# Kernel optimization log

Hardware: AMD Instinct MI355X
Metric: run time of the kernel (lower is better)

## Reference

```python
import jax, jax.numpy as jnp
import numpy as np

N_P, N_A = 100000, 20000
F_P, D_A, H = 512, 128, 256
E_W, E_C = 200000, 400000


def setup_inputs() -> dict:
    key = jax.random.key(0)
    ks = jax.random.split(key, 32)
    s = 0.05  # param init scale
    inp = {
        # node inputs
        'paper_feat': (jax.random.uniform(ks[0], (N_P, F_P)) < 0.02).astype(jnp.float32),  # sparse multi-hot
        'author_emb': jax.random.normal(ks[1], (N_A, D_A), jnp.float32),
        # edges: author --writes--> paper, paper --cites--> paper
        'writes_src': jax.random.randint(ks[2], (E_W,), 0, N_A, jnp.int32),
        'writes_dst': jax.random.randint(ks[3], (E_W,), 0, N_P, jnp.int32),
        'writes_w': jax.random.uniform(ks[4], (E_W,), jnp.float32),
        'cites_src': jax.random.randint(ks[5], (E_C,), 0, N_P, jnp.int32),
        'cites_dst': jax.random.randint(ks[6], (E_C,), 0, N_P, jnp.int32),
        'cites_w': jax.random.uniform(ks[7], (E_C,), jnp.float32),
        # layer 1 params (in dims per node type: paper=F_P, author=D_A)
        'W1_self_p': jax.random.normal(ks[8], (F_P, H), jnp.float32) * s,
        'b1_self_p': jnp.zeros((H,), jnp.float32),
        'W1_self_a': jax.random.normal(ks[9], (D_A, H), jnp.float32) * s,
        'b1_self_a': jnp.zeros((H,), jnp.float32),
        'W1_rel_writes': jax.random.normal(ks[10], (D_A, H), jnp.float32) * s,
        'b1_rel_writes': jnp.zeros((H,), jnp.float32),
        'W1_rel_cites': jax.random.normal(ks[11], (F_P, H), jnp.float32) * s,
        'b1_rel_cites': jnp.zeros((H,), jnp.float32),
        # layer 2 params (all in dims = H)
        'W2_self_p': jax.random.normal(ks[12], (H, H), jnp.float32) * s,
        'b2_self_p': jnp.zeros((H,), jnp.float32),
        'W2_self_a': jax.random.normal(ks[13], (H, H), jnp.float32) * s,
        'b2_self_a': jnp.zeros((H,), jnp.float32),
        'W2_rel_writes': jax.random.normal(ks[14], (H, H), jnp.float32) * s,
        'b2_rel_writes': jnp.zeros((H,), jnp.float32),
        'W2_rel_cites': jax.random.normal(ks[15], (H, H), jnp.float32) * s,
        'b2_rel_cites': jnp.zeros((H,), jnp.float32),
    }
    return inp


def _hetero_layer(xp, xa, edges, Wsp, bsp, Wsa, bsa, Wrw, brw, Wrc, brc, activation):
    """One HeteroLayer: per-type self linear + per-relation gather/scale/scatter-add."""
    writes_src, writes_dst, writes_w, cites_src, cites_dst, cites_w = edges
    out_p = xp @ Wsp + bsp          # [N_P, H]
    out_a = xa @ Wsa + bsa          # [N_A, H]
    # relation author --writes--> paper
    msg_w = xa @ Wrw + brw          # dense per-relation linear on source nodes
    gathered_w = msg_w[writes_src] * writes_w[:, None]          # gather + edge weight
    out_p = out_p + jax.ops.segment_sum(gathered_w, writes_dst, num_segments=out_p.shape[0])
    # relation paper --cites--> paper
    msg_c = xp @ Wrc + brc
    gathered_c = msg_c[cites_src] * cites_w[:, None]
    out_p = out_p + jax.ops.segment_sum(gathered_c, cites_dst, num_segments=out_p.shape[0])
    if activation:
        out_p = jax.nn.elu(out_p)
        out_a = jax.nn.elu(out_a)
    return out_p, out_a


def reference(paper_feat, author_emb,
              writes_src, writes_dst, writes_w,
              cites_src, cites_dst, cites_w,
              W1_self_p, b1_self_p, W1_self_a, b1_self_a,
              W1_rel_writes, b1_rel_writes, W1_rel_cites, b1_rel_cites,
              W2_self_p, b2_self_p, W2_self_a, b2_self_a,
              W2_rel_writes, b2_rel_writes, W2_rel_cites, b2_rel_cites):
    edges = (writes_src, writes_dst, writes_w, cites_src, cites_dst, cites_w)
    xp, xa = _hetero_layer(paper_feat, author_emb, edges,
                           W1_self_p, b1_self_p, W1_self_a, b1_self_a,
                           W1_rel_writes, b1_rel_writes, W1_rel_cites, b1_rel_cites,
                           activation=True)
    xp, xa = _hetero_layer(xp, xa, edges,
                           W2_self_p, b2_self_p, W2_self_a, b2_self_a,
                           W2_rel_writes, b2_rel_writes, W2_rel_cites, b2_rel_cites,
                           activation=False)
    return xp, xa
```

## Files before the change

kernel.cpp:

```cpp
#include <hip/hip_runtime.h>
#include <cstdint>
#include <cstddef>

constexpr int Hd  = 256;
constexpr int N_P = 100000;
constexpr int N_A = 20000;
constexpr int F_P = 512;
constexpr int D_A = 128;

typedef short bf16x8 __attribute__((ext_vector_type(8)));
typedef float f32x4  __attribute__((ext_vector_type(4)));

__device__ __forceinline__ unsigned short f2b(float x) {
    unsigned u = __float_as_uint(x);
    u += 0x7fffu + ((u >> 16) & 1u);
    return (unsigned short)(u >> 16);
}
__device__ __forceinline__ float b2f(unsigned short h) {
    return __uint_as_float((unsigned)h << 16);
}
__device__ __forceinline__ unsigned pk2(float lo, float hi) {
    return (__float_as_uint(lo) >> 16) | (__float_as_uint(hi) & 0xffff0000u);
}

__device__ __forceinline__ void bsplit(float x, unsigned short& hi, unsigned short& lo) {
    const unsigned u = __float_as_uint(x);
    hi = (unsigned short)(u >> 16);
    const float r = x - __uint_as_float(u & 0xffff0000u);
    lo = (unsigned short)(__float_as_uint(r) >> 16);
}

__global__ void prep_kernel(const float* __restrict__ W1sa, const float* __restrict__ W1rw,
                            const float* __restrict__ W2sa, const float* __restrict__ W2rw,
                            const float* __restrict__ W2rc, const float* __restrict__ W2sp,
                            const float* __restrict__ W1sp, const float* __restrict__ W1rc,
                            const float* __restrict__ b1sa, const float* __restrict__ b1rw,
                            const float* __restrict__ b2sa, const float* __restrict__ b2rw,
                            const float* __restrict__ b2rc, const float* __restrict__ b2sp,
                            const float* __restrict__ b1sp, const float* __restrict__ b1rc,
                            unsigned short* __restrict__ w1h,  unsigned short* __restrict__ w1l,
                            unsigned short* __restrict__ wA2h, unsigned short* __restrict__ wA2l,
                            unsigned short* __restrict__ wP2h,
                            unsigned short* __restrict__ wP1h,
                            float* __restrict__ bc1, float* __restrict__ bcA2,
                            float* __restrict__ bcP2, float* __restrict__ bcP1) {
    const int b = blockIdx.x;
    const int l = threadIdx.x;
    if (b < 384) {
        const float *Wa, *Wb; unsigned short *wh, *wl; int rel;
        if (b < 128) { Wa = W1sa; Wb = W1rw; wh = w1h;  wl = w1l;  rel = b; }
        else         { Wa = W2sa; Wb = W2rw; wh = wA2h; wl = wA2l; rel = b - 128; }
        const int ks  = rel >> 5;
        const int nfg = rel & 31;
        const float* W = (nfg < 16) ? Wa : Wb;
        const int col  = (nfg & 15) * 16 + (l & 15);
        const size_t base = ((size_t)rel * 64 + l) * 8;
        #pragma unroll
        for (int j = 0; j < 8; ++j) {
            const int k = ks * 32 + ((l >> 4) * 8) + j;
            unsigned short h, lw;
            bsplit(W[(size_t)k * Hd + col], h, lw);
            wh[base + j] = h;
            wl[base + j] = lw;
        }
    } else if (b < 640) {
        const int rel = b - 384;
        const int ks  = rel >> 5;
        const int nfg = rel & 31;
        const float* W = (nfg < 16) ? W2rc : W2sp;
        const int col  = (nfg & 15) * 16 + (l & 15);
        const size_t base = ((size_t)rel * 64 + l) * 8;
        #pragma unroll
        for (int j = 0; j < 8; ++j) {
            const int k = ks * 32 + ((l >> 4) * 8) + j;
            wP2h[base + j] = f2b(W[(size_t)k * Hd + col]);
        }
    } else if (b < 1152) {
        const int rel = b - 640;
        const int ks  = rel >> 5;
        const int nfg = rel & 31;
        const float* W = (nfg < 16) ? W1sp : W1rc;
        const int col  = (nfg & 15) * 16 + (l & 15);
        const size_t base = ((size_t)rel * 64 + l) * 8;
        #pragma unroll
        for (int j = 0; j < 8; ++j) {
            const int k = ks * 32 + ((l >> 4) * 8) + j;
            wP1h[base + j] = f2b(W[(size_t)k * Hd + col]);
        }
    } else {
        const int t     = (b - 1152) * 64 + l;
        const int which = t >> 9;
        const int idx   = t & 511;
        const float* src; float* dst;
        if (which == 0)      { src = (idx < 256) ? b1sa : b1rw; dst = bc1;  }
        else if (which == 1) { src = (idx < 256) ? b2sa : b2rw; dst = bcA2; }
        else if (which == 2) { src = (idx < 256) ? b2rc : b2sp; dst = bcP2; }
        else                 { src = (idx < 256) ? b1sp : b1rc; dst = bcP1; }
        dst[idx] = src[idx & 255];
    }
}

template<int ASRC>
__global__ void __launch_bounds__(256, 3)
mfma_tile_kernel(const void* __restrict__ Av, const int KA, const int nks,
                 const unsigned short* __restrict__ wtab,
                 const float* __restrict__ bcat,
                 void* __restrict__ Oa, void* __restrict__ Ob,
                 const int bfA, const int bfB, const int Mtot) {
    extern __shared__ char smem[];
    const int tid = threadIdx.x;
    const int wid = tid >> 6;
    const int l   = tid & 63;
    const int c   = blockIdx.x & 3;
    const long m0 = (long)(blockIdx.x >> 2) * 128;
    const int wr  = wid >> 1, wc = wid & 1;

    const int f0 = tid >> 6;
    const int le = tid & 63;
    long grow0 = m0 + f0 * 16 + (le & 15);       if (grow0 > Mtot - 1) grow0 = Mtot - 1;
    long grow1 = m0 + (f0 + 4) * 16 + (le & 15); if (grow1 > Mtot - 1) grow1 = Mtot - 1;
    const int kg = (le >> 4) * 8;

    float4 a00, a01, a10, a11;
    uint4  ua0, ua1;
    uint4  ub0, ub1;

#define TK_LOAD(KS) { \
    if constexpr (ASRC == 0) { \
        const float* A = (const float*)Av; \
        const float* p0_ = A + grow0 * KA + (KS) * 32 + kg; \
        const float* p1_ = A + grow1 * KA + (KS) * 32 + kg; \
        a00 = *(const float4*)p0_; a01 = *(const float4*)(p0_ + 4); \
        a10 = *(const float4*)p1_; a11 = *(const float4*)(p1_ + 4); \
    } else { \
        const unsigned short* A = (const unsigned short*)Av; \
        ua0 = *(const uint4*)(A + grow0 * KA + (KS) * 32 + kg); \
        ua1 = *(const uint4*)(A + grow1 * KA + (KS) * 32 + kg); \
    } \
    { const unsigned short* bs_ = wtab + ((size_t)((KS) * 32 + c * 8) * 512) + tid * 16; \
      ub0 = *(const uint4*)bs_; ub1 = *(const uint4*)(bs_ + 8); } }

#define TK_WRITE(BUF) { \
    char* Ab_ = smem + (BUF) * 16384; \
    char* Bb_ = Ab_ + 8192; \
    if constexpr (ASRC == 0) { \
        *(uint4*)(Ab_ + tid * 16) = make_uint4(pk2(a00.x, a00.y), pk2(a00.z, a00.w), \
                                               pk2(a01.x, a01.y), pk2(a01.z, a01.w)); \
        *(uint4*)(Ab_ + (tid + 256) * 16) = make_uint4(pk2(a10.x, a10.y), pk2(a10.z, a10.w), \
                                                       pk2(a11.x, a11.y), pk2(a11.z, a11.w)); \
    } else { \
        *(uint4*)(Ab_ + tid * 16) = ua0; \
        *(uint4*)(Ab_ + (tid + 256) * 16) = ua1; \
    } \
    *(uint4*)(Bb_ + tid * 32) = ub0; \
    *(uint4*)(Bb_ + tid * 32 + 16) = ub1; }

    f32x4 acc[4][4];
    #pragma unroll
    for (int nf = 0; nf < 4; ++nf) {
        const float b = bcat[c * 128 + wc * 64 + nf * 16 + (l & 15)];
        #pragma unroll
        for (int mf = 0; mf < 4; ++mf) acc[mf][nf] = (f32x4){b, b, b, b};
    }

    TK_LOAD(0)
    TK_WRITE(0)
    __syncthreads();

    int cur = 0;
    for (int ks = 0; ks < nks; ++ks) {
        const bool more = (ks + 1 < nks);
        if (more) TK_LOAD(ks + 1)
        {
            const char* Ab = smem + cur * 16384;
            const char* Bb = Ab + 8192;
            bf16x8 af[4], bfv[4];
            #pragma unroll
            for (int mf = 0; mf < 4; ++mf)
                af[mf] = *(const bf16x8*)(Ab + ((wr * 4 + mf) * 64 + l) * 16);
            #pragma unroll
            for (int nf = 0; nf < 4; ++nf)
                bfv[nf] = *(const bf16x8*)(Bb + ((wc * 4 + nf) * 64 + l) * 16);
            #pragma unroll
            for (int nf = 0; nf < 4; ++nf) {
                #pragma unroll
                for (int mf = 0; mf < 4; ++mf)
                    acc[mf][nf] = __builtin_amdgcn_mfma_f32_16x16x32_bf16(af[mf], bfv[nf], acc[mf][nf], 0, 0, 0);
            }
        }
        if (more) TK_WRITE(cur ^ 1)
        __syncthreads();
        cur ^= 1;
    }
#undef TK_LOAD
#undef TK_WRITE

    #pragma unroll
    for (int mf = 0; mf < 4; ++mf) {
        #pragma unroll
        for (int nf = 0; nf < 4; ++nf) {
            const int gcol = c * 128 + wc * 64 + nf * 16 + (l & 15);
            void* O; int col, isbf;
            if (gcol < 256) { O = Oa; col = gcol;       isbf = bfA; }
            else            { O = Ob; col = gcol - 256; isbf = bfB; }
            const long row = m0 + wr * 64 + mf * 16 + ((l >> 4) * 4);
            const f32x4 v = acc[mf][nf];
            #pragma unroll
            for (int r = 0; r < 4; ++r) {
                if (row + r < Mtot) {
                    const float x = v[r];
                    if (isbf) ((unsigned short*)O)[(row + r) * Hd + col] = f2b(x);
                    else      ((float*)O)[(row + r) * Hd + col] = x;
                }
            }
        }
    }
}

__global__ void mfma_dual_kernel(const void* __restrict__ Av, const int K,
                                 const unsigned short* __restrict__ whi,
                                 const unsigned short* __restrict__ wlo,
                                 const float* __restrict__ bcat,
                                 void* __restrict__ Oa, void* __restrict__ Ob,
                                 const int actA, const int actB,
                                 const int bfA, const int bfB) {
    extern __shared__ char smem[];
    char* sh = smem;
    char* sl = smem + 32 * K * 2;
    const int  tid = threadIdx.x;
    const int  wid = tid >> 6;
    const int  l   = tid & 63;
    const long m0  = (long)blockIdx.x * 32;
    const int  rowStride = 2 * K;

    const int kq4 = K >> 2;
    const float* A = (const float*)Av;
    for (int i = tid; i < 32 * kq4; i += 256) {
        const int row = i / kq4;
        const int kq  = i - row * kq4;
        const float4 v = *(const float4*)(A + (m0 + row) * K + kq * 4);
        unsigned short h0, h1, h2, h3, l0, l1, l2, l3;
        bsplit(v.x, h0, l0); bsplit(v.y, h1, l1);
        bsplit(v.z, h2, l2); bsplit(v.w, h3, l3);
        const int ofs = row * rowStride + ((kq * 8) ^ ((row & 7) << 4));
        *(ushort4*)(sh + ofs) = make_ushort4(h0, h1, h2, h3);
        *(ushort4*)(sl + ofs) = make_ushort4(l0, l1, l2, l3);
    }
    __syncthreads();

    f32x4 acc[2][8];
    #pragma unroll
    for (int nf = 0; nf < 8; ++nf) {
        const float b = bcat[wid * 128 + nf * 16 + (l & 15)];
        acc[0][nf] = (f32x4){b, b, b, b};
        acc[1][nf] = (f32x4){b, b, b, b};
    }

    const int kb  = (l >> 4) * 16;
    const int r0  = l & 15;
    const int r1  = 16 + r0;
    const int sw  = (l & 7) << 4;
    const int ro0 = r0 * rowStride;
    const int ro1 = r1 * rowStride;
    for (int ks = 0; ks < (K >> 5); ++ks) {
        const int bk = (ks * 64 + kb) ^ sw;
        const bf16x8 ah0 = *(const bf16x8*)(sh + ro0 + bk);
        const bf16x8 ah1 = *(const bf16x8*)(sh + ro1 + bk);
        const bf16x8 al0 = *(const bf16x8*)(sl + ro0 + bk);
        const bf16x8 al1 = *(const bf16x8*)(sl + ro1 + bk);
        const size_t wbase = (((size_t)ks * 32 + wid * 8) * 64 + l) * 8;
        #pragma unroll
        for (int nf = 0; nf < 8; ++nf) {
            const bf16x8 bh = *(const bf16x8*)(whi + wbase + (size_t)nf * 512);
            const bf16x8 bl = *(const bf16x8*)(wlo + wbase + (size_t)nf * 512);
            acc[0][nf] = __builtin_amdgcn_mfma_f32_16x16x32_bf16(ah0, bh, acc[0][nf], 0, 0, 0);
            acc[1][nf] = __builtin_amdgcn_mfma_f32_16x16x32_bf16(ah1, bh, acc[1][nf], 0, 0, 0);
            acc[0][nf] = __builtin_amdgcn_mfma_f32_16x16x32_bf16(al0, bh, acc[0][nf], 0, 0, 0);
            acc[1][nf] = __builtin_amdgcn_mfma_f32_16x16x32_bf16(al1, bh, acc[1][nf], 0, 0, 0);
            acc[0][nf] = __builtin_amdgcn_mfma_f32_16x16x32_bf16(ah0, bl, acc[0][nf], 0, 0, 0);
            acc[1][nf] = __builtin_amdgcn_mfma_f32_16x16x32_bf16(ah1, bl, acc[1][nf], 0, 0, 0);
        }
    }

    #pragma unroll
    for (int mf = 0; mf < 2; ++mf) {
        #pragma unroll
        for (int nf = 0; nf < 8; ++nf) {
            const int colg = wid * 128 + nf * 16 + (l & 15);
            void* O;
            int col, act, isbf;
            if (colg < 256) { O = Oa; col = colg;       act = actA; isbf = bfA; }
            else            { O = Ob; col = colg - 256; act = actB; isbf = bfB; }
            const long row = m0 + mf * 16 + ((l >> 4) * 4);
            const f32x4 v = acc[mf][nf];
            #pragma unroll
            for (int r = 0; r < 4; ++r) {
                float x = v[r];
                if (act) x = x > 0.f ? x : expm1f(x);
                if (isbf) ((unsigned short*)O)[(row + r) * Hd + col] = f2b(x);
                else      ((float*)O)[(row + r) * Hd + col] = x;
            }
        }
    }
}

__global__ void hist_kernel(const int* __restrict__ wdst, const int EW,
                            const int* __restrict__ cdst, const int EC,
                            int* __restrict__ cnt) {
    for (int i = blockIdx.x * blockDim.x + threadIdx.x; i < EW + EC; i += gridDim.x * blockDim.x) {
        const int d = (i < EW) ? wdst[i] : cdst[i - EW];
        atomicAdd(&cnt[d], 1);
    }
}

__global__ void scan1_kernel(int* __restrict__ data, const int n, int* __restrict__ bsum) {
    __shared__ int s[256];
    const int t = threadIdx.x;
    const int base = blockIdx.x * 1024 + t * 4;
    int v0 = (base + 0 < n) ? data[base + 0] : 0;
    int v1 = (base + 1 < n) ? data[base + 1] : 0;
    int v2 = (base + 2 < n) ? data[base + 2] : 0;
    int v3 = (base + 3 < n) ? data[base + 3] : 0;
    const int tsum = v0 + v1 + v2 + v3;
    s[t] = tsum;
    __syncthreads();
    for (int off = 1; off < 256; off <<= 1) {
        int y = (t >= off) ? s[t - off] : 0;
        __syncthreads();
        if (t >= off) s[t] += y;
        __syncthreads();
    }
    const int e = s[t] - tsum;
    if (base + 0 < n) data[base + 0] = e;
    if (base + 1 < n) data[base + 1] = e + v0;
    if (base + 2 < n) data[base + 2] = e + v0 + v1;
    if (base + 3 < n) data[base + 3] = e + v0 + v1 + v2;
    if (t == 255) bsum[blockIdx.x] = s[255];
}

__global__ void scan2_kernel(int* __restrict__ bsum, const int nb) {
    __shared__ int s[256];
    const int t = threadIdx.x;
    const int v = (t < nb) ? bsum[t] : 0;
    s[t] = v;
    __syncthreads();
    for (int off = 1; off < 256; off <<= 1) {
        int y = (t >= off) ? s[t - off] : 0;
        __syncthreads();
        if (t >= off) s[t] += y;
        __syncthreads();
    }
    if (t < nb) bsum[t] = s[t] - v;
}

__global__ void scan3_kernel(int* __restrict__ data, const int n, const int* __restrict__ bsum) {
    const int i = blockIdx.x * blockDim.x + threadIdx.x;
    if (i < n) data[i] += bsum[i >> 10];
}

__global__ void fill_kernel(const int* __restrict__ wsrc, const int* __restrict__ wdst,
                            const float* __restrict__ ww, const int EW,
                            const int* __restrict__ csrc, const int* __restrict__ cdst,
                            const float* __restrict__ cw, const int EC,
                            int* __restrict__ cur, int2* __restrict__ edges) {
    for (int i = blockIdx.x * blockDim.x + threadIdx.x; i < EW + EC; i += gridDim.x * blockDim.x) {
        int d, sp; float w;
        if (i < EW) { d = wdst[i]; sp = wsrc[i]; w = ww[i]; }
        else        { const int j = i - EW; d = cdst[j]; sp = N_A + csrc[j]; w = cw[j]; }
        const int p = atomicAdd(&cur[d], 1);
        edges[p] = make_int2(sp, __float_as_int(w));
    }
}

struct AgChunk { ushort4 g0, g1, g2, g3; float w0, w1, w2, w3; };

__device__ __forceinline__ void ag_issue(const int2* __restrict__ eq, const int base, const int n,
                                         const unsigned short* __restrict__ msg,
                                         const int lane, AgChunk& C) {
#define AG_ONE(J, GG, WW) { \
    const int idx = base + (J); \
    const int2 ee = eq[min(idx, n - 1)]; \
    WW = (idx < n) ? __int_as_float(ee.y) : 0.f; \
    GG = ((const ushort4*)(msg + (size_t)ee.x * Hd))[lane]; }
    AG_ONE(0, C.g0, C.w0)
    AG_ONE(1, C.g1, C.w1)
    AG_ONE(2, C.g2, C.w2)
    AG_ONE(3, C.g3, C.w3)
#undef AG_ONE
}

__device__ __forceinline__ void ag_acc(const AgChunk& C, float4& acc) {
#define AG_A(GG, WW) { \
    acc.x = fmaf(WW, b2f(GG.x), acc.x); acc.y = fmaf(WW, b2f(GG.y), acc.y); \
    acc.z = fmaf(WW, b2f(GG.z), acc.z); acc.w = fmaf(WW, b2f(GG.w), acc.w); }
    AG_A(C.g0, C.w0) AG_A(C.g1, C.w1) AG_A(C.g2, C.w2) AG_A(C.g3, C.w3)
#undef AG_A
}

template<int IOBF>
__global__ void aggregate_kernel(void* __restrict__ iov,
                                 const unsigned short* __restrict__ msgAll,
                                 const int* __restrict__ off,
                                 const int2* __restrict__ edges,
                                 const int do_elu) {
    __shared__ int2 eq[1024];
    const int wid  = threadIdx.x >> 6;
    const int lane = threadIdx.x & 63;
    const int p0   = blockIdx.x * 4;
    const int sAll = (p0 == 0) ? 0 : off[p0 - 1];
    const int tot  = off[p0 + 3] - sAll;
    const bool fits = (tot <= 1024);
    if (fits)
        for (int i = threadIdx.x; i < tot; i += 256) eq[i] = edges[sAll + i];
    __syncthreads();

    const int p = p0 + wid;
    const int s = (p == 0) ? 0 : off[p - 1];
    const int e = off[p];
    const int n = e - s;

    float4 acc;
    if constexpr (IOBF) {
        const ushort4 t = ((const ushort4*)((const unsigned short*)iov + (size_t)p * Hd))[lane];
        acc = make_float4(b2f(t.x), b2f(t.y), b2f(t.z), b2f(t.w));
    } else {
        acc = ((const float4*)((const float*)iov + (size_t)p * Hd))[lane];
    }

    if (n > 0) {
        if (fits) {
            const int2* eqw = eq + (s - sAll);
            int nc = (n + 3) >> 2;
            nc += (nc & 1);
            AgChunk CA, CB;
            ag_issue(eqw, 0, n, msgAll, lane, CA);
            int c = 1;
            for (; c + 1 < nc; c += 2) {
                ag_issue(eqw, 4 * c, n, msgAll, lane, CB);
                ag_acc(CA, acc);
                ag_issue(eqw, 4 * (c + 1), n, msgAll, lane, CA);
                ag_acc(CB, acc);
            }
            ag_issue(eqw, 4 * (nc - 1), n, msgAll, lane, CB);
            ag_acc(CA, acc);
            ag_acc(CB, acc);
        } else {
            for (int i = s; i < e; ++i) {
                const int2 ee = edges[i];
                const ushort4 g = ((const ushort4*)(msgAll + (size_t)ee.x * Hd))[lane];
                const float w = __int_as_float(ee.y);
                acc.x = fmaf(w, b2f(g.x), acc.x); acc.y = fmaf(w, b2f(g.y), acc.y);
                acc.z = fmaf(w, b2f(g.z), acc.z); acc.w = fmaf(w, b2f(g.w), acc.w);
            }
        }
    }
    if (do_elu) {
        acc.x = acc.x > 0.f ? acc.x : expm1f(acc.x);
        acc.y = acc.y > 0.f ? acc.y : expm1f(acc.y);
        acc.z = acc.z > 0.f ? acc.z : expm1f(acc.z);
        acc.w = acc.w > 0.f ? acc.w : expm1f(acc.w);
    }
    if constexpr (IOBF) {
        ((ushort4*)((unsigned short*)iov + (size_t)p * Hd))[lane] =
            make_ushort4(f2b(acc.x), f2b(acc.y), f2b(acc.z), f2b(acc.w));
    } else {
        ((float4*)((float*)iov + (size_t)p * Hd))[lane] = acc;
    }
}

extern "C" void kernel_launch(void* const* d_in, const int* in_sizes, int n_in,
                              void* d_out, int out_size, void* d_ws, size_t ws_size,
                              hipStream_t stream) {
    const float* pf    = (const float*)d_in[0];
    const float* ae    = (const float*)d_in[1];
    const int*   wsrc  = (const int*)d_in[2];
    const int*   wdst  = (const int*)d_in[3];
    const float* ww    = (const float*)d_in[4];
    const int*   csrc  = (const int*)d_in[5];
    const int*   cdst  = (const int*)d_in[6];
    const float* cw    = (const float*)d_in[7];
    const float* W1sp  = (const float*)d_in[8];
    const float* b1sp  = (const float*)d_in[9];
    const float* W1sa  = (const float*)d_in[10];
    const float* b1sa  = (const float*)d_in[11];
    const float* W1rw  = (const float*)d_in[12];
    const float* b1rw  = (const float*)d_in[13];
    const float* W1rc  = (const float*)d_in[14];
    const float* b1rc  = (const float*)d_in[15];
    const float* W2sp  = (const float*)d_in[16];
    const float* b2sp  = (const float*)d_in[17];
    const float* W2sa  = (const float*)d_in[18];
    const float* b2sa  = (const float*)d_in[19];
    const float* W2rw  = (const float*)d_in[20];
    const float* b2rw  = (const float*)d_in[21];
    const float* W2rc  = (const float*)d_in[22];
    const float* b2rc  = (const float*)d_in[23];

    const int E_W = in_sizes[2];
    const int E_C = in_sizes[5];

    float* outP = (float*)d_out;
    float* outA = outP + (size_t)N_P * Hd;

    float*          xa1    = (float*)d_ws;
    unsigned short* xp1b   = (unsigned short*)(xa1 + (size_t)N_A * Hd);
    unsigned short* msgAll = xp1b + (size_t)N_P * Hd;
    unsigned short* msgP   = msgAll + (size_t)N_A * Hd;
    int*            off    = (int*)(msgAll + (size_t)(N_A + N_P) * Hd);
    int2*           edges  = (int2*)(off + N_P);
    int*            bsum   = (int*)(edges + (E_W + E_C));
    float*          bc1    = (float*)(bsum + 256);
    float*          bcA2   = bc1 + 512;
    float*          bcP2   = bcA2 + 512;
    float*          bcP1   = bcP2 + 512;
    unsigned short* w1h    = (unsigned short*)(bcP1 + 512);
    unsigned short* w1l    = w1h  + (size_t)128 * 512;
    unsigned short* wA2h   = w1l  + (size_t)128 * 512;
    unsigned short* wA2l   = wA2h + (size_t)256 * 512;
    unsigned short* wP2h   = wA2l + (size_t)256 * 512;
    unsigned short* wP1h   = wP2h + (size_t)256 * 512;

    const dim3 blk(256);
    const int  nb  = (N_P + 1023) / 1024;
    const int  gM  = (N_P + 127) / 128;
    const int  gP  = gM * 4;

    prep_kernel<<<1184, 64, 0, stream>>>(W1sa, W1rw, W2sa, W2rw, W2rc, W2sp, W1sp, W1rc,
                                         b1sa, b1rw, b2sa, b2rw, b2rc, b2sp, b1sp, b1rc,
                                         w1h, w1l, wA2h, wA2l, wP2h, wP1h,
                                         bc1, bcA2, bcP2, bcP1);

    hipMemsetAsync(off, 0, (size_t)N_P * sizeof(int), stream);
    hist_kernel<<<1024, blk, 0, stream>>>(wdst, E_W, cdst, E_C, off);
    scan1_kernel<<<nb, blk, 0, stream>>>(off, N_P, bsum);
    scan2_kernel<<<1,  blk, 0, stream>>>(bsum, nb);
    scan3_kernel<<<(N_P + 255) / 256, blk, 0, stream>>>(off, N_P, bsum);
    fill_kernel<<<1024, blk, 0, stream>>>(wsrc, wdst, ww, E_W, csrc, cdst, cw, E_C,
                                          off, edges);

    mfma_tile_kernel<0><<<gP, blk, 32768, stream>>>(pf, 512, 16, wP1h, bcP1,
                                                    xp1b, msgP, 1, 1, N_P);
    mfma_dual_kernel<<<N_A / 32, blk, 32 * 128 * 4, stream>>>(ae, 128, w1h, w1l, bc1,
                                                              xa1, msgAll, 1, 0, 0, 1);
    aggregate_kernel<1><<<N_P / 4, blk, 0, stream>>>(xp1b, msgAll, off, edges, 1);

    mfma_dual_kernel<<<N_A / 32, blk, 32 * 256 * 4, stream>>>(xa1, 256, wA2h, wA2l, bcA2,
                                                              outA, msgAll, 0, 0, 0, 1);
    mfma_tile_kernel<1><<<gP, blk, 32768, stream>>>(xp1b, 256, 8, wP2h, bcP2,
                                                    msgP, outP, 1, 0, N_P);
    aggregate_kernel<0><<<N_P / 4, blk, 0, stream>>>(outP, msgAll, off, edges, 0);
}
```

Measured before the change: 504.9 us.

## Stage GEMM tiles via global_load_lds and pre-convert paper features to bf16

The MFMA tile kernel now stages its B operand and its bf16 A operand directly from global memory into LDS with global_load_lds, which removes the register round-trip and the explicit LDS stores. When the workspace is large enough, a separate kernel first converts paper_feat from fp32 to bf16 by truncation, so the layer-1 GEMM can also use direct LDS staging. The conversion adds a full extra read of the fp32 input plus a bf16 write. Each of the four column-tile blocks then reads half the bytes it read before.

Result: faster. 476.2 us (-5.7%).

```diff
diff --git a/kernel.cpp b/kernel.cpp
--- a/kernel.cpp
+++ b/kernel.cpp
@@ -22,12 +22,17 @@
 __device__ __forceinline__ unsigned pk2(float lo, float hi) {
     return (__float_as_uint(lo) >> 16) | (__float_as_uint(hi) & 0xffff0000u);
 }
-
 __device__ __forceinline__ void bsplit(float x, unsigned short& hi, unsigned short& lo) {
     const unsigned u = __float_as_uint(x);
     hi = (unsigned short)(u >> 16);
     const float r = x - __uint_as_float(u & 0xffff0000u);
     lo = (unsigned short)(__float_as_uint(r) >> 16);
+}
+
+__device__ __forceinline__ void gld16(const void* g, void* l) {
+    __builtin_amdgcn_global_load_lds(
+        (const __attribute__((address_space(1))) unsigned int*)g,
+        (__attribute__((address_space(3))) unsigned int*)l, 16, 0, 0);
 }
 
 __global__ void prep_kernel(const float* __restrict__ W1sa, const float* __restrict__ W1rw,
@@ -100,13 +105,26 @@
     }
 }
 
-template<int ASRC>
+__global__ void conv_kernel(const float* __restrict__ in, unsigned short* __restrict__ out,
+                            const long n4) {
+    const long stride = (long)gridDim.x * blockDim.x;
+    for (long i = (long)blockIdx.x * blockDim.x + threadIdx.x; i < n4; i += stride) {
+        const float4 v = ((const float4*)in)[i];
+        ((ushort4*)out)[i] = make_ushort4(
+            (unsigned short)(__float_as_uint(v.x) >> 16),
+            (unsigned short)(__float_as_uint(v.y) >> 16),
+            (unsigned short)(__float_as_uint(v.z) >> 16),
+            (unsigned short)(__float_as_uint(v.w) >> 16));
+    }
+}
+
+template<int AMODE>
 __global__ void __launch_bounds__(256, 3)
-mfma_tile_kernel(const void* __restrict__ Av, const int KA, const int nks,
-                 const unsigned short* __restrict__ wtab,
-                 const float* __restrict__ bcat,
-                 void* __restrict__ Oa, void* __restrict__ Ob,
-                 const int bfA, const int bfB, const int Mtot) {
+mfma_tile2_kernel(const void* __restrict__ Av, const int KA, const int nks,
+                  const unsigned short* __restrict__ wtab,
+                  const float* __restrict__ bcat,
+                  void* __restrict__ Oa, void* __restrict__ Ob,
+                  const int bfA, const int bfB, const int Mtot) {
     extern __shared__ char smem[];
     const int tid = threadIdx.x;
     const int wid = tid >> 6;
@@ -115,45 +133,47 @@
     const long m0 = (long)(blockIdx.x >> 2) * 128;
     const int wr  = wid >> 1, wc = wid & 1;
 
-    const int f0 = tid >> 6;
-    const int le = tid & 63;
-    long grow0 = m0 + f0 * 16 + (le & 15);       if (grow0 > Mtot - 1) grow0 = Mtot - 1;
-    long grow1 = m0 + (f0 + 4) * 16 + (le & 15); if (grow1 > Mtot - 1) grow1 = Mtot - 1;
-    const int kg = (le >> 4) * 8;
+    const unsigned short* bg0 = wtab + ((size_t)(c * 8 + 2 * wid) * 512) + l * 8;
+    const unsigned short* bg1 = bg0 + 512;
+
+    const unsigned short* ag0 = nullptr; const unsigned short* ag1 = nullptr;
+    const float* Af = nullptr;
+    long grow0 = 0, grow1 = 0; int kg = 0;
+    if constexpr (AMODE == 1) {
+        const unsigned short* A = (const unsigned short*)Av;
+        long r0 = m0 + (2 * wid) * 16 + (l & 15);     if (r0 > Mtot - 1) r0 = Mtot - 1;
+        long r1 = m0 + (2 * wid + 1) * 16 + (l & 15); if (r1 > Mtot - 1) r1 = Mtot - 1;
+        ag0 = A + r0 * KA + ((l >> 4) * 8);
+        ag1 = A + r1 * KA + ((l >> 4) * 8);
+    } else {
+        Af = (const float*)Av;
+        const int f0 = tid >> 6;
+        grow0 = m0 + f0 * 16 + (l & 15);       if (grow0 > Mtot - 1) grow0 = Mtot - 1;
+        grow1 = m0 + (f0 + 4) * 16 + (l & 15); if (grow1 > Mtot - 1) grow1 = Mtot - 1;
+        kg = (l >> 4) * 8;
+    }
 
     float4 a00, a01, a10, a11;
-    uint4  ua0, ua1;
-    uint4  ub0, ub1;
-
-#define TK_LOAD(KS) { \
-    if constexpr (ASRC == 0) { \
-        const float* A = (const float*)Av; \
-        const float* p0_ = A + grow0 * KA + (KS) * 32 + kg; \
-        const float* p1_ = A + grow1 * KA + (KS) * 32 + kg; \
-        a00 = *(const float4*)p0_; a01 = *(const float4*)(p0_ + 4); \
-        a10 = *(const float4*)p1_; a11 = *(const float4*)(p1_ + 4); \
-    } else { \
-        const unsigned short* A = (const unsigned short*)Av; \
-        ua0 = *(const uint4*)(A + grow0 * KA + (KS) * 32 + kg); \
-        ua1 = *(const uint4*)(A + grow1 * KA + (KS) * 32 + kg); \
-    } \
-    { const unsigned short* bs_ = wtab + ((size_t)((KS) * 32 + c * 8) * 512) + tid * 16; \
-      ub0 = *(const uint4*)bs_; ub1 = *(const uint4*)(bs_ + 8); } }
-
-#define TK_WRITE(BUF) { \
+
+#define STAGE_B(BUF, KS) { \
+    char* Bb_ = smem + (BUF) * 16384 + 8192; \
+    gld16(bg0 + (size_t)(KS) * 16384, Bb_ + wid * 2048); \
+    gld16(bg1 + (size_t)(KS) * 16384, Bb_ + wid * 2048 + 1024); }
+#define STAGE_A1(BUF, KS) { \
     char* Ab_ = smem + (BUF) * 16384; \
-    char* Bb_ = Ab_ + 8192; \
-    if constexpr (ASRC == 0) { \
-        *(uint4*)(Ab_ + tid * 16) = make_uint4(pk2(a00.x, a00.y), pk2(a00.z, a00.w), \
-                                               pk2(a01.x, a01.y), pk2(a01.z, a01.w)); \
-        *(uint4*)(Ab_ + (tid + 256) * 16) = make_uint4(pk2(a10.x, a10.y), pk2(a10.z, a10.w), \
-                                                       pk2(a11.x, a11.y), pk2(a11.z, a11.w)); \
-    } else { \
-        *(uint4*)(Ab_ + tid * 16) = ua0; \
-        *(uint4*)(Ab_ + (tid + 256) * 16) = ua1; \
-    } \
-    *(uint4*)(Bb_ + tid * 32) = ub0; \
-    *(uint4*)(Bb_ + tid * 32 + 16) = ub1; }
+    gld16(ag0 + (KS) * 32, Ab_ + wid * 2048); \
+    gld16(ag1 + (KS) * 32, Ab_ + wid * 2048 + 1024); }
+#define LOAD_A0(KS) { \
+    const float* p0_ = Af + grow0 * KA + (KS) * 32 + kg; \
+    const float* p1_ = Af + grow1 * KA + (KS) * 32 + kg; \
+    a00 = *(const float4*)p0_; a01 = *(const float4*)(p0_ + 4); \
+    a10 = *(const float4*)p1_; a11 = *(const float4*)(p1_ + 4); }
+#define WRITE_A0(BUF) { \
+    char* Ab_ = smem + (BUF) * 16384; \
+    *(uint4*)(Ab_ + tid * 16) = make_uint4(pk2(a00.x, a00.y), pk2(a00.z, a00.w), \
+                                           pk2(a01.x, a01.y), pk2(a01.z, a01.w)); \
+    *(uint4*)(Ab_ + (tid + 256) * 16) = make_uint4(pk2(a10.x, a10.y), pk2(a10.z, a10.w), \
+                                                   pk2(a11.x, a11.y), pk2(a11.z, a11.w)); }
 
     f32x4 acc[4][4];
     #pragma unroll
@@ -163,14 +183,19 @@
         for (int mf = 0; mf < 4; ++mf) acc[mf][nf] = (f32x4){b, b, b, b};
     }
 
-    TK_LOAD(0)
-    TK_WRITE(0)
+    STAGE_B(0, 0)
+    if constexpr (AMODE == 1) { STAGE_A1(0, 0) }
+    else { LOAD_A0(0) WRITE_A0(0) }
     __syncthreads();
 
     int cur = 0;
     for (int ks = 0; ks < nks; ++ks) {
         const bool more = (ks + 1 < nks);
-        if (more) TK_LOAD(ks + 1)
+        if (more) {
+            STAGE_B(cur ^ 1, ks + 1)
+            if constexpr (AMODE == 1) { STAGE_A1(cur ^ 1, ks + 1) }
+            else { LOAD_A0(ks + 1) }
+        }
         {
             const char* Ab = smem + cur * 16384;
             const char* Bb = Ab + 8192;
@@ -188,12 +213,14 @@
                     acc[mf][nf] = __builtin_amdgcn_mfma_f32_16x16x32_bf16(af[mf], bfv[nf], acc[mf][nf], 0, 0, 0);
             }
         }
-        if (more) TK_WRITE(cur ^ 1)
+        if (more) { if constexpr (AMODE == 0) WRITE_A0(cur ^ 1) }
         __syncthreads();
         cur ^= 1;
     }
-#undef TK_LOAD
-#undef TK_WRITE
+#undef STAGE_B
+#undef STAGE_A1
+#undef LOAD_A0
+#undef WRITE_A0
 
     #pragma unroll
     for (int mf = 0; mf < 4; ++mf) {
@@ -519,6 +546,10 @@
     unsigned short* wA2l   = wA2h + (size_t)256 * 512;
     unsigned short* wP2h   = wA2l + (size_t)256 * 512;
     unsigned short* wP1h   = wP2h + (size_t)256 * 512;
+    unsigned short* pfb    = (unsigned short*)
+        (((uintptr_t)(wP1h + (size_t)512 * 512) + 63) & ~(uintptr_t)63);
+    const size_t need = ((char*)(pfb + (size_t)N_P * F_P)) - (char*)d_ws;
+    const bool usePfb = (ws_size >= need);
 
     const dim3 blk(256);
     const int  nb  = (N_P + 1023) / 1024;
@@ -538,15 +569,21 @@
     fill_kernel<<<1024, blk, 0, stream>>>(wsrc, wdst, ww, E_W, csrc, cdst, cw, E_C,
                                           off, edges);
 
-    mfma_tile_kernel<0><<<gP, blk, 32768, stream>>>(pf, 512, 16, wP1h, bcP1,
-                                                    xp1b, msgP, 1, 1, N_P);
+    if (usePfb) {
+        conv_kernel<<<2048, blk, 0, stream>>>(pf, pfb, (long)N_P * F_P / 4);
+        mfma_tile2_kernel<1><<<gP, blk, 32768, stream>>>(pfb, 512, 16, wP1h, bcP1,
+                                                         xp1b, msgP, 1, 1, N_P);
+    } else {
+        mfma_tile2_kernel<0><<<gP, blk, 32768, stream>>>(pf, 512, 16, wP1h, bcP1,
+                                                         xp1b, msgP, 1, 1, N_P);
+    }
     mfma_dual_kernel<<<N_A / 32, blk, 32 * 128 * 4, stream>>>(ae, 128, w1h, w1l, bc1,
                                                               xa1, msgAll, 1, 0, 0, 1);
     aggregate_kernel<1><<<N_P / 4, blk, 0, stream>>>(xp1b, msgAll, off, edges, 1);
 
     mfma_dual_kernel<<<N_A / 32, blk, 32 * 256 * 4, stream>>>(xa1, 256, wA2h, wA2l, bcA2,
                                                               outA, msgAll, 0, 0, 0, 1);
-    mfma_tile_kernel<1><<<gP, blk, 32768, stream>>>(xp1b, 256, 8, wP2h, bcP2,
-                                                    msgP, outP, 1, 0, N_P);
+    mfma_tile2_kernel<1><<<gP, blk, 32768, stream>>>(xp1b, 256, 8, wP2h, bcP2,
+                                                     msgP, outP, 1, 0, N_P);
     aggregate_kernel<0><<<N_P / 4, blk, 0, stream>>>(outP, msgAll, off, edges, 0);
 }
```
